# Performance work log

Measured on AMD Instinct MI355X. Metric: run time of the kernel, lower is better.

## Reference

```python
import jax, jax.numpy as jnp
import numpy as np
import math

B, TSRC, TTGT, DM, DI, H = 2, 2048, 2048, 1024, 1024, 16
DH = DI // H
LN_EPS = 1e-5


def setup_inputs() -> dict:
    key = jax.random.key(0)
    ks = iter(jax.random.split(key, 40))
    def p(*shape):
        return jax.random.normal(next(ks), shape, jnp.float32) * 0.02
    inp = {
        "enc_out_vecs": jax.random.normal(next(ks), (B, TSRC, DM), jnp.float32),
        "output_vecs": jax.random.normal(next(ks), (B, TTGT, DM), jnp.float32),
    }
    for tag in ("dd", "ed"):
        inp["Wq_" + tag] = p(DM, DI); inp["bq_" + tag] = jnp.zeros((DI,), jnp.float32)
        inp["Wk_" + tag] = p(DM, DI); inp["bk_" + tag] = jnp.zeros((DI,), jnp.float32)
        inp["Wv_" + tag] = p(DM, DI); inp["bv_" + tag] = jnp.zeros((DI,), jnp.float32)
        inp["Wo_" + tag] = p(DI, DM); inp["bo_" + tag] = jnp.zeros((DM,), jnp.float32)
        inp["W1_" + tag] = p(DM, 2 * DM); inp["b1_" + tag] = jnp.zeros((2 * DM,), jnp.float32)
        inp["W2_" + tag] = p(2 * DM, DM); inp["b2_" + tag] = jnp.zeros((DM,), jnp.float32)
        inp["g1_" + tag] = jnp.ones((DM,), jnp.float32); inp["be1_" + tag] = jnp.zeros((DM,), jnp.float32)
        inp["g2_" + tag] = jnp.ones((DM,), jnp.float32); inp["be2_" + tag] = jnp.zeros((DM,), jnp.float32)
    return inp


def _ln(x, g, b):
    m = jnp.mean(x, axis=-1, keepdims=True)
    v = jnp.var(x, axis=-1, keepdims=True)
    return (x - m) * jax.lax.rsqrt(v + LN_EPS) * g + b


def _mha(xq, xkv, Wq, bq, Wk, bk, Wv, bv, causal):
    Bb, Tq, _ = xq.shape
    Tk = xkv.shape[1]
    q = (xq @ Wq + bq).reshape(Bb, Tq, H, DH)
    k = (xkv @ Wk + bk).reshape(Bb, Tk, H, DH)
    v = (xkv @ Wv + bv).reshape(Bb, Tk, H, DH)
    s = jnp.einsum("bqhd,bkhd->bhqk", q, k) / math.sqrt(DH)
    if causal:
        mask = jnp.where(jnp.arange(Tk)[None, :] > jnp.arange(Tq)[:, None], -jnp.inf, 0.0)
        s = s + mask
    w = jax.nn.softmax(s, axis=-1)
    return jnp.einsum("bhqk,bkhd->bqhd", w, v).reshape(Bb, Tq, H * DH)


def reference(enc_out_vecs, output_vecs,
              Wq_dd, bq_dd, Wk_dd, bk_dd, Wv_dd, bv_dd, Wo_dd, bo_dd,
              W1_dd, b1_dd, W2_dd, b2_dd, g1_dd, be1_dd, g2_dd, be2_dd,
              Wq_ed, bq_ed, Wk_ed, bk_ed, Wv_ed, bv_ed, Wo_ed, bo_ed,
              W1_ed, b1_ed, W2_ed, b2_ed, g1_ed, be1_ed, g2_ed, be2_ed):
    # masked self-attention over decoder inputs
    x = output_vecs
    a = _mha(x, x, Wq_dd, bq_dd, Wk_dd, bk_dd, Wv_dd, bv_dd, causal=True)
    x = _ln(a @ Wo_dd + bo_dd + x, g1_dd, be1_dd)
    x = _ln(x + jax.nn.relu(x @ W1_dd + b1_dd) @ W2_dd + b2_dd, g2_dd, be2_dd)
    # cross attention against encoder outputs
    a = _mha(x, enc_out_vecs, Wq_ed, bq_ed, Wk_ed, bk_ed, Wv_ed, bv_ed, causal=False)
    x = _ln(a @ Wo_ed + bo_ed + x, g1_ed, be1_ed)
    x = _ln(jax.nn.relu(x @ W1_ed + b1_ed) @ W2_ed + b2_ed + x, g2_ed, be2_ed)
    return x
```

## Files before the change

kernel.cpp:

```cpp
#include <hip/hip_runtime.h>
#include <stdint.h>

#define DEV __device__ __forceinline__
typedef unsigned short u16;
typedef __attribute__((ext_vector_type(8))) short bf16x8;
typedef __attribute__((ext_vector_type(4))) float f32x4;

#define AS1 __attribute__((address_space(1)))
#define AS3 __attribute__((address_space(3)))
#define WAITVM0 asm volatile("s_waitcnt vmcnt(0)" ::: "memory")
#define QSCALE 0.18033688011112042f

DEV u16 f2bf(float f) {
  union { float f; uint32_t u; } x; x.f = f;
  uint32_t r = x.u + 0x7fffu + ((x.u >> 16) & 1u);
  return (u16)(r >> 16);
}

DEV float bf2f(u16 h) {
  union { uint32_t u; float f; } x; x.u = ((uint32_t)h) << 16;
  return x.f;
}

DEV uint32_t cvt_pk_bf16(float a, float b) {
  uint32_t r;
  asm("v_cvt_pk_bf16_f32 %0, %1, %2" : "=v"(r) : "v"(a), "v"(b));
  return r;
}

struct WTJob { const float* W; u16* WT; int K, M, msh, start; };
struct WTJobs { WTJob j[12]; };

__global__ __launch_bounds__(256) void k_init(WTJobs jobs, int wtBlocks,
                                              const float* __restrict__ a, const float* __restrict__ bsrc,
                                              u16* __restrict__ oa, u16* __restrict__ ob, int n4) {
  __shared__ float tile[32][33];
  int b = blockIdx.x;
  int tid = threadIdx.x;
  if (b >= wtBlocks) {
    int i = (b - wtBlocks) * 256 + tid;
    const float* s;
    u16* o;
    int k;
    if (i < n4) { s = a; o = oa; k = i; }
    else        { s = bsrc; o = ob; k = i - n4; }
    float4 v = reinterpret_cast<const float4*>(s)[k];
    reinterpret_cast<ushort4*>(o)[k] = make_ushort4(f2bf(v.x), f2bf(v.y), f2bf(v.z), f2bf(v.w));
    return;
  }
  int i = 0;
#pragma unroll
  for (int t = 1; t < 12; ++t)
    if (b >= jobs.j[t].start) i = t;
  const WTJob J = jobs.j[i];
  int rel = b - J.start;
  int m0 = (rel & ((1 << J.msh) - 1)) << 5;
  int k0 = (rel >> J.msh) << 5;
  int tx = tid & 31, ty = tid >> 5;
#pragma unroll
  for (int q = 0; q < 4; ++q)
    tile[ty + q * 8][tx] = J.W[(size_t)(k0 + ty + q * 8) * J.M + m0 + tx];
  __syncthreads();
#pragma unroll
  for (int q = 0; q < 4; ++q)
    J.WT[(size_t)(m0 + ty + q * 8) * J.K + k0 + tx] = f2bf(tile[tx][ty + q * 8]);
}

template<int R>
DEV void stage_tile(const u16* __restrict__ g, int strideElems, u16* lds, int tid, int wv) {
#pragma unroll
  for (int t = 0; t < R / 32; ++t) {
    int idx = t * 256 + tid;
    int row = idx >> 3;
    int b = (idx & 7) << 4;
    int sb = b ^ ((row & 7) << 4);
    const char* src = (const char*)g + (size_t)row * strideElems * 2 + sb;
    char* dst = (char*)lds + (size_t)(t * 256 + wv * 64) * 16;
    __builtin_amdgcn_global_load_lds((const AS1 void*)src, (AS3 void*)dst, 16, 0, 0);
  }
}

DEV bf16x8 lds_frag(const u16* lds, int row, int kel) {
  int off = row * 128 + ((kel * 2) ^ ((row & 7) << 4));
  return *(const bf16x8*)((const char*)lds + off);
}

template<int JT, int MODE>
__global__ __launch_bounds__(256) void k_gemm(const u16* __restrict__ A, int lda,
                                              const u16* __restrict__ BT,
                                              const float* __restrict__ bias,
                                              u16* __restrict__ C, int ldc, int K) {
  constexpr int BN = JT * 32;
  __shared__ __align__(16) u16 A_lds[2][128 * 64];
  __shared__ __align__(16) u16 B_lds[2][BN * 64];
  const int tid = threadIdx.x, lane = tid & 63, wv = tid >> 6;
  const int wm = wv >> 1, wn = wv & 1;
  const int nwg = gridDim.x * gridDim.y;
  const int flat = blockIdx.y * gridDim.x + blockIdx.x;
  const int sw = (flat & 7) * (nwg >> 3) + (flat >> 3);
  const int bx = sw % gridDim.x, by = sw / gridDim.x;
  const int bm0 = by * 128, bn0 = bx * BN;
  const int lr = lane & 15, lk = (lane >> 4) * 8, r0 = (lane >> 4) * 4;

  f32x4 acc[4][JT];
#pragma unroll
  for (int i = 0; i < 4; ++i)
#pragma unroll
    for (int j = 0; j < JT; ++j) acc[i][j] = f32x4{0.f, 0.f, 0.f, 0.f};

  stage_tile<128>(A + (size_t)bm0 * lda, lda, A_lds[0], tid, wv);
  stage_tile<BN>(BT + (size_t)bn0 * K, K, B_lds[0], tid, wv);
  WAITVM0;
  __builtin_amdgcn_s_barrier();

  int cur = 0;
  for (int k0 = 0; k0 < K; k0 += 64) {
    if (k0 + 64 < K) {
      stage_tile<128>(A + (size_t)bm0 * lda + k0 + 64, lda, A_lds[cur ^ 1], tid, wv);
      stage_tile<BN>(BT + (size_t)bn0 * K + k0 + 64, K, B_lds[cur ^ 1], tid, wv);
    }
#pragma unroll
    for (int kk = 0; kk < 2; ++kk) {
      bf16x8 af[4], bfr[JT];
#pragma unroll
      for (int i = 0; i < 4; ++i) af[i] = lds_frag(A_lds[cur], wm * 64 + i * 16 + lr, kk * 32 + lk);
#pragma unroll
      for (int j = 0; j < JT; ++j) bfr[j] = lds_frag(B_lds[cur], wn * (JT * 16) + j * 16 + lr, kk * 32 + lk);
#pragma unroll
      for (int i = 0; i < 4; ++i)
#pragma unroll
        for (int j = 0; j < JT; ++j)
          acc[i][j] = __builtin_amdgcn_mfma_f32_16x16x32_bf16(af[i], bfr[j], acc[i][j], 0, 0, 0);
    }
    WAITVM0;
    __builtin_amdgcn_s_barrier();
    cur ^= 1;
  }

#pragma unroll
  for (int j = 0; j < JT; ++j) {
    int col = bn0 + wn * (JT * 16) + j * 16 + lr;
    float bv = bias[col];
#pragma unroll
    for (int i = 0; i < 4; ++i) {
      int rowb = bm0 + wm * 64 + i * 16 + r0;
#pragma unroll
      for (int r = 0; r < 4; ++r) {
        float v = acc[i][j][r] + bv;
        if constexpr (MODE == 2) v = fmaxf(v, 0.f);
        C[(size_t)(rowb + r) * ldc + col] = f2bf(v);
      }
    }
  }
}

__global__ __launch_bounds__(256) void k_qkv(const u16* __restrict__ Aq, const u16* __restrict__ Akv,
                                             const u16* __restrict__ BT,
                                             const float* __restrict__ bq, const float* __restrict__ bk,
                                             const float* __restrict__ bv,
                                             u16* __restrict__ Qb, u16* __restrict__ Kb,
                                             u16* __restrict__ Vt, int K) {
  __shared__ __align__(16) u16 A_lds[2][128 * 64];
  __shared__ __align__(16) u16 B_lds[2][128 * 64];
  const int tid = threadIdx.x, lane = tid & 63, wv = tid >> 6;
  const int wm = wv >> 1, wn = wv & 1;
  const int nwg = gridDim.x * gridDim.y;
  const int flat = blockIdx.y * gridDim.x + blockIdx.x;
  const int sw = (flat & 7) * (nwg >> 3) + (flat >> 3);
  const int bx = sw % gridDim.x, by = sw / gridDim.x;
  const int bm0 = by * 128, bn0 = bx * 128;
  const int seg = bn0 >> 10;
  const u16* A = (seg == 0) ? Aq : Akv;
  const int lr = lane & 15, lk = (lane >> 4) * 8, r0 = (lane >> 4) * 4;

  f32x4 acc[4][4];
#pragma unroll
  for (int i = 0; i < 4; ++i)
#pragma unroll
    for (int j = 0; j < 4; ++j) acc[i][j] = f32x4{0.f, 0.f, 0.f, 0.f};

  stage_tile<128>(A + (size_t)bm0 * K, K, A_lds[0], tid, wv);
  stage_tile<128>(BT + (size_t)bn0 * K, K, B_lds[0], tid, wv);
  WAITVM0;
  __builtin_amdgcn_s_barrier();

  int cur = 0;
  for (int k0 = 0; k0 < K; k0 += 64) {
    if (k0 + 64 < K) {
      stage_tile<128>(A + (size_t)bm0 * K + k0 + 64, K, A_lds[cur ^ 1], tid, wv);
      stage_tile<128>(BT + (size_t)bn0 * K + k0 + 64, K, B_lds[cur ^ 1], tid, wv);
    }
#pragma unroll
    for (int kk = 0; kk < 2; ++kk) {
      bf16x8 af[4], bfr[4];
#pragma unroll
      for (int i = 0; i < 4; ++i) af[i] = lds_frag(A_lds[cur], wm * 64 + i * 16 + lr, kk * 32 + lk);
#pragma unroll
      for (int j = 0; j < 4; ++j) bfr[j] = lds_frag(B_lds[cur], wn * 64 + j * 16 + lr, kk * 32 + lk);
#pragma unroll
      for (int i = 0; i < 4; ++i)
#pragma unroll
        for (int j = 0; j < 4; ++j)
          acc[i][j] = __builtin_amdgcn_mfma_f32_16x16x32_bf16(af[i], bfr[j], acc[i][j], 0, 0, 0);
    }
    WAITVM0;
    __builtin_amdgcn_s_barrier();
    cur ^= 1;
  }

#pragma unroll
  for (int j = 0; j < 4; ++j) {
    int col = bn0 + wn * 64 + j * 16 + lr;
    int cl = col & 1023;
#pragma unroll
    for (int i = 0; i < 4; ++i) {
      int rowb = bm0 + wm * 64 + i * 16 + r0;
      if (seg == 0) {
        float bb = bq[cl];
#pragma unroll
        for (int r = 0; r < 4; ++r)
          Qb[(size_t)(rowb + r) * 1024 + cl] = f2bf((acc[i][j][r] + bb) * QSCALE);
      } else if (seg == 1) {
        float bb = bk[cl];
#pragma unroll
        for (int r = 0; r < 4; ++r)
          Kb[(size_t)(rowb + r) * 1024 + cl] = f2bf(acc[i][j][r] + bb);
      } else {
        float bb = bv[cl];
        int bidx = rowb >> 11, t = rowb & 2047;
        ushort4 o = make_ushort4(f2bf(acc[i][j][0] + bb), f2bf(acc[i][j][1] + bb),
                                 f2bf(acc[i][j][2] + bb), f2bf(acc[i][j][3] + bb));
        *reinterpret_cast<ushort4*>(&Vt[((size_t)bidx * 1024 + cl) * 2048 + t]) = o;
      }
    }
  }
}

__global__ __launch_bounds__(256) void k_ln_b(const u16* __restrict__ Rm, const u16* __restrict__ X,
                                              const float* __restrict__ g, const float* __restrict__ be,
                                              u16* __restrict__ Yb, float* __restrict__ Yf) {
  int row = blockIdx.x;
  size_t base4 = (size_t)row * 256;
  int t = threadIdx.x;
  ushort4 a4 = reinterpret_cast<const ushort4*>(Rm)[base4 + t];
  ushort4 x4 = reinterpret_cast<const ushort4*>(X)[base4 + t];
  float v0 = bf2f(a4.x) + bf2f(x4.x), v1 = bf2f(a4.y) + bf2f(x4.y);
  float v2 = bf2f(a4.z) + bf2f(x4.z), v3 = bf2f(a4.w) + bf2f(x4.w);
  float s = v0 + v1 + v2 + v3;
  float ss = v0 * v0 + v1 * v1 + v2 * v2 + v3 * v3;
#pragma unroll
  for (int m = 1; m < 64; m <<= 1) { s += __shfl_xor(s, m); ss += __shfl_xor(ss, m); }
  __shared__ float red[8];
  int wv = t >> 6;
  if ((t & 63) == 0) { red[wv] = s; red[4 + wv] = ss; }
  __syncthreads();
  s = red[0] + red[1] + red[2] + red[3];
  ss = red[4] + red[5] + red[6] + red[7];
  float mean = s * (1.f / 1024.f);
  float var = ss * (1.f / 1024.f) - mean * mean;
  float rstd = rsqrtf(var + 1e-5f);
  float4 gv = reinterpret_cast<const float4*>(g)[t];
  float4 bv = reinterpret_cast<const float4*>(be)[t];
  float o0 = (v0 - mean) * rstd * gv.x + bv.x;
  float o1 = (v1 - mean) * rstd * gv.y + bv.y;
  float o2 = (v2 - mean) * rstd * gv.z + bv.z;
  float o3 = (v3 - mean) * rstd * gv.w + bv.w;
  if (Yb) {
    ushort4 ob = make_ushort4(f2bf(o0), f2bf(o1), f2bf(o2), f2bf(o3));
    reinterpret_cast<ushort4*>(Yb)[base4 + t] = ob;
  }
  if (Yf)
    reinterpret_cast<float4*>(Yf)[base4 + t] = make_float4(o0, o1, o2, o3);
}

template<bool CAUSAL>
__global__ __launch_bounds__(512) void k_attn(const u16* __restrict__ Q, const u16* __restrict__ Kg,
                                              const u16* __restrict__ Vt, u16* __restrict__ O, int T) {
  __shared__ __align__(16) u16 K_lds[3][64 * 64];
  __shared__ __align__(16) u16 V_lds[3][64 * 64];
  __shared__ __align__(16) u16 p_lds[8][16 * 64];
  const int tid = threadIdx.x, lane = tid & 63, wv = tid >> 6;
  const int h = blockIdx.y, b = blockIdx.z;
  const int lq = lane & 15, g = lane >> 4;
  const int swz = (lq & 7) << 4;
  const int fb0 = lq * 128 + ((g * 16) ^ swz);
  const int fb1 = lq * 128 + ((g * 16 + 64) ^ swz);
  const size_t qkbase = ((size_t)b * T) * 1024 + h * 64;
  const size_t vbase = ((size_t)b * 1024 + h * 64) * T;

  const int qx = CAUSAL ? (gridDim.x - 1 - blockIdx.x) : blockIdx.x;
  const int en = CAUSAL ? (2 * qx + 2) : (T >> 6);
  const int qw = qx * 128 + wv * 16;
  const int dtile = qw >> 6;

  bf16x8 aq0, aq1;
  {
    const u16* qp_ = Q + qkbase + (size_t)(qw + lq) * 1024 + g * 8;
    aq0 = *reinterpret_cast<const bf16x8*>(qp_);
    aq1 = *reinterpret_cast<const bf16x8*>(qp_ + 32);
  }

  const int srow = tid >> 3;
  const int ssb = ((tid & 7) << 4) ^ ((srow & 7) << 4);
  const char* ksrc = (const char*)(Kg + qkbase) + (size_t)srow * 2048 + ssb;
  const char* vsrc = (const char*)(Vt + vbase) + (size_t)srow * ((size_t)T * 2) + ssb;
  const uint32_t doff = (uint32_t)(wv << 10);

  auto stage = [&](int buf) {
    __builtin_amdgcn_global_load_lds((const AS1 void*)ksrc, (AS3 void*)((char*)K_lds[buf] + doff), 16, 0, 0);
    __builtin_amdgcn_global_load_lds((const AS1 void*)vsrc, (AS3 void*)((char*)V_lds[buf] + doff), 16, 0, 0);
    ksrc += 131072;
    vsrc += 128;
  };

  f32x4 acc[4];
  float lsum = 0.f;
#pragma unroll
  for (int j = 0; j < 4; ++j) acc[j] = f32x4{0.f, 0.f, 0.f, 0.f};

  char* pw = (char*)p_lds[wv];

  auto qstep = [&](bool domask, int kv0, const char* kb, const char* vb) {
    f32x4 st_[4];
    __builtin_amdgcn_s_setprio(1);
#pragma unroll
    for (int j = 0; j < 4; ++j) {
      bf16x8 bk0 = *reinterpret_cast<const bf16x8*>(kb + fb0 + j * 2048);
      bf16x8 bk1 = *reinterpret_cast<const bf16x8*>(kb + fb1 + j * 2048);
      f32x4 t0 = f32x4{0.f, 0.f, 0.f, 0.f};
      t0 = __builtin_amdgcn_mfma_f32_16x16x32_bf16(bk0, aq0, t0, 0, 0, 0);
      t0 = __builtin_amdgcn_mfma_f32_16x16x32_bf16(bk1, aq1, t0, 0, 0, 0);
      st_[j] = t0;
    }
    __builtin_amdgcn_s_setprio(0);
    uint32_t pk[8];
    if (domask) {
      const int qrow = qw + lq;
#pragma unroll
      for (int j = 0; j < 4; ++j) {
        float p0 = __builtin_exp2f(st_[j][0]);
        float p1 = __builtin_exp2f(st_[j][1]);
        float p2 = __builtin_exp2f(st_[j][2]);
        float p3 = __builtin_exp2f(st_[j][3]);
        int kvb = kv0 + j * 16 + g * 4;
        p0 = (kvb > qrow) ? 0.f : p0;
        p1 = (kvb + 1 > qrow) ? 0.f : p1;
        p2 = (kvb + 2 > qrow) ? 0.f : p2;
        p3 = (kvb + 3 > qrow) ? 0.f : p3;
        lsum += (p0 + p1) + (p2 + p3);
        pk[2 * j] = cvt_pk_bf16(p0, p1);
        pk[2 * j + 1] = cvt_pk_bf16(p2, p3);
      }
    } else {
#pragma unroll
      for (int j = 0; j < 4; ++j) {
        float p0 = __builtin_exp2f(st_[j][0]);
        float p1 = __builtin_exp2f(st_[j][1]);
        float p2 = __builtin_exp2f(st_[j][2]);
        float p3 = __builtin_exp2f(st_[j][3]);
        lsum += (p0 + p1) + (p2 + p3);
        pk[2 * j] = cvt_pk_bf16(p0, p1);
        pk[2 * j + 1] = cvt_pk_bf16(p2, p3);
      }
    }
#pragma unroll
    for (int j = 0; j < 4; ++j)
      *reinterpret_cast<uint2*>(pw + lq * 128 + ((j * 32 + g * 8) ^ swz)) =
          make_uint2(pk[2 * j], pk[2 * j + 1]);
    bf16x8 pf0 = *reinterpret_cast<const bf16x8*>(pw + fb0);
    bf16x8 pf1 = *reinterpret_cast<const bf16x8*>(pw + fb1);
    __builtin_amdgcn_s_setprio(1);
#pragma unroll
    for (int j2 = 0; j2 < 4; ++j2) {
      bf16x8 v0 = *reinterpret_cast<const bf16x8*>(vb + fb0 + j2 * 2048);
      bf16x8 v1 = *reinterpret_cast<const bf16x8*>(vb + fb1 + j2 * 2048);
      acc[j2] = __builtin_amdgcn_mfma_f32_16x16x32_bf16(v0, pf0, acc[j2], 0, 0, 0);
      acc[j2] = __builtin_amdgcn_mfma_f32_16x16x32_bf16(v1, pf1, acc[j2], 0, 0, 0);
    }
    __builtin_amdgcn_s_setprio(0);
  };

  stage(0);
  if (en > 1) {
    stage(1);
    asm volatile("s_waitcnt vmcnt(2)" ::: "memory");
  } else {
    WAITVM0;
  }
  __builtin_amdgcn_s_barrier();

  for (int it = 0; it < en; ++it) {
    if (it + 2 < en) stage((it + 2) % 3);
    const char* kb = (const char*)K_lds[it % 3];
    const char* vb = (const char*)V_lds[it % 3];
    if (!CAUSAL || it <= dtile)
      qstep(CAUSAL && it == dtile, it << 6, kb, vb);
    if (it + 2 < en) {
      asm volatile("s_waitcnt vmcnt(2)" ::: "memory");
    } else {
      WAITVM0;
    }
    __builtin_amdgcn_s_barrier();
  }

  lsum += __shfl_xor(lsum, 16);
  lsum += __shfl_xor(lsum, 32);
  float inv = 1.f / lsum;
  size_t rb = qkbase + (size_t)(qw + lq) * 1024;
#pragma unroll
  for (int j2 = 0; j2 < 4; ++j2) {
    ushort4 o = make_ushort4(f2bf(acc[j2][0] * inv), f2bf(acc[j2][1] * inv),
                             f2bf(acc[j2][2] * inv), f2bf(acc[j2][3] * inv));
    *reinterpret_cast<ushort4*>(&O[rb + j2 * 16 + g * 4]) = o;
  }
}

extern "C" void kernel_launch(void* const* d_in, const int* in_sizes, int n_in,
                              void* d_out, int out_size, void* d_ws, size_t ws_size,
                              hipStream_t stream) {
  const int T = 2048;
  const float* enc = (const float*)d_in[0];
  const float* outv = (const float*)d_in[1];
  auto F = [&](int i) { return (const float*)d_in[i]; };

  size_t off = 0;
  auto alloc = [&](size_t bytes) {
    void* p = (char*)d_ws + off;
    off += (bytes + 255) & ~(size_t)255;
    return p;
  };

  const int tdK[12] = {1024, 1024, 1024, 1024, 1024, 2048, 1024, 1024, 1024, 1024, 1024, 2048};
  const int tdM[12] = {1024, 1024, 1024, 1024, 2048, 1024, 1024, 1024, 1024, 1024, 2048, 1024};
  const int tdIdx[12] = {2, 4, 6, 8, 10, 12, 18, 20, 22, 24, 26, 28};
  u16* WT_[12];
  for (int i = 0; i < 12; ++i) WT_[i] = (u16*)alloc((size_t)tdK[i] * tdM[i] * 2);

  u16* Xb0 = (u16*)alloc(4096ull * 1024 * 2);
  u16* Eb = (u16*)alloc(4096ull * 1024 * 2);
  u16* Qb = (u16*)alloc(4096ull * 1024 * 2);
  u16* Kb = (u16*)alloc(4096ull * 1024 * 2);
  u16* Vt = (u16*)alloc(4096ull * 1024 * 2);
  u16* Ab = (u16*)alloc(4096ull * 1024 * 2);
  u16* Hb = (u16*)alloc(4096ull * 2048 * 2);
  u16* Rm = (u16*)alloc(4096ull * 1024 * 2);
  u16* X1b = (u16*)alloc(4096ull * 1024 * 2);
  u16* X2b = (u16*)alloc(4096ull * 1024 * 2);
  u16* X3b = (u16*)alloc(4096ull * 1024 * 2);

  WTJobs jobs;
  int start = 0;
  for (int i = 0; i < 12; ++i) {
    int msh = (tdM[i] == 2048) ? 6 : 5;
    jobs.j[i] = {F(tdIdx[i]), WT_[i], tdK[i], tdM[i], msh, start};
    start += (tdM[i] >> 5) * (tdK[i] >> 5);
  }
  const int n4 = 4096 * 1024 / 4;
  k_init<<<start + 8192, 256, 0, stream>>>(jobs, start, outv, enc, Xb0, Eb, n4);

  dim3 gq(24, 32);
  dim3 g1k(16, 32);
  dim3 g2k(16, 32);
  dim3 ga(16, 16, 2);

  k_qkv<<<gq, 256, 0, stream>>>(Xb0, Xb0, WT_[0], F(3), F(5), F(7), Qb, Kb, Vt, 1024);
  k_attn<true><<<ga, 512, 0, stream>>>(Qb, Kb, Vt, Ab, T);
  k_gemm<2, 1><<<g1k, 256, 0, stream>>>(Ab, 1024, WT_[3], F(9), Rm, 1024, 1024);
  k_ln_b<<<4096, 256, 0, stream>>>(Rm, Xb0, F(14), F(15), X1b, nullptr);
  k_gemm<4, 2><<<g2k, 256, 0, stream>>>(X1b, 1024, WT_[4], F(11), Hb, 2048, 1024);
  k_gemm<2, 1><<<g1k, 256, 0, stream>>>(Hb, 2048, WT_[5], F(13), Rm, 1024, 2048);
  k_ln_b<<<4096, 256, 0, stream>>>(Rm, X1b, F(16), F(17), X2b, nullptr);

  k_qkv<<<gq, 256, 0, stream>>>(X2b, Eb, WT_[6], F(19), F(21), F(23), Qb, Kb, Vt, 1024);
  k_attn<false><<<ga, 512, 0, stream>>>(Qb, Kb, Vt, Ab, T);
  k_gemm<2, 1><<<g1k, 256, 0, stream>>>(Ab, 1024, WT_[9], F(25), Rm, 1024, 1024);
  k_ln_b<<<4096, 256, 0, stream>>>(Rm, X2b, F(30), F(31), X3b, nullptr);
  k_gemm<4, 2><<<g2k, 256, 0, stream>>>(X3b, 1024, WT_[10], F(27), Hb, 2048, 1024);
  k_gemm<2, 1><<<g1k, 256, 0, stream>>>(Hb, 2048, WT_[11], F(29), Rm, 1024, 2048);
  k_ln_b<<<4096, 256, 0, stream>>>(Rm, X3b, F(32), F(33), nullptr, (float*)d_out);
}
```

Before: 412.6 us.

## Overlap cross-attention K/V projection with causal self-attention in one launch

After: 396.9 us. -3.8%, faster.

```diff
diff --git a/kernel.cpp b/kernel.cpp
--- a/kernel.cpp
+++ b/kernel.cpp
@@ -80,6 +80,20 @@
   }
 }
 
+template<int R>
+DEV void stage512(const u16* __restrict__ g, int strideElems, u16* lds, int tid, int wv) {
+#pragma unroll
+  for (int t = 0; t < R / 64; ++t) {
+    int idx = t * 512 + tid;
+    int row = idx >> 3;
+    int b = (idx & 7) << 4;
+    int sb = b ^ ((row & 7) << 4);
+    const char* src = (const char*)g + (size_t)row * strideElems * 2 + sb;
+    char* dst = (char*)lds + (size_t)(t * 512 + wv * 64) * 16;
+    __builtin_amdgcn_global_load_lds((const AS1 void*)src, (AS3 void*)dst, 16, 0, 0);
+  }
+}
+
 DEV bf16x8 lds_frag(const u16* lds, int row, int kel) {
   int off = row * 128 + ((kel * 2) ^ ((row & 7) << 4));
   return *(const bf16x8*)((const char*)lds + off);
@@ -148,6 +162,7 @@
       for (int r = 0; r < 4; ++r) {
         float v = acc[i][j][r] + bv;
         if constexpr (MODE == 2) v = fmaxf(v, 0.f);
+        if constexpr (MODE == 3) v = v * QSCALE;
         C[(size_t)(rowb + r) * ldc + col] = f2bf(v);
       }
     }
@@ -415,6 +430,221 @@
   }
 }
 
+__global__ __launch_bounds__(512) void k_attn_kv(const u16* __restrict__ Q, const u16* __restrict__ Kg,
+                                                 const u16* __restrict__ Vt, u16* __restrict__ O, int T,
+                                                 const u16* __restrict__ Eb, const u16* __restrict__ BT2,
+                                                 const float* __restrict__ bk2, const float* __restrict__ bv2,
+                                                 u16* __restrict__ Kb2, u16* __restrict__ Vt2) {
+  __shared__ __align__(16) char smem[81920];
+  const int tid = threadIdx.x, lane = tid & 63, wv = tid >> 6;
+
+  if (blockIdx.x < 512) {
+    const int a = blockIdx.x;
+    const int b = a >> 8, h = (a >> 4) & 15, qi = a & 15;
+    const int qx = 15 - qi;
+    const int en = 2 * qx + 2;
+    const int lq = lane & 15, g = lane >> 4;
+    const int swz = (lq & 7) << 4;
+    const int fb0 = lq * 128 + ((g * 16) ^ swz);
+    const int fb1 = lq * 128 + ((g * 16 + 64) ^ swz);
+    const size_t qkbase = ((size_t)b * T) * 1024 + h * 64;
+    const size_t vbase = ((size_t)b * 1024 + h * 64) * T;
+    const int qw = qx * 128 + wv * 16;
+    const int dtile = qw >> 6;
+
+    char* Kl = smem;
+    char* Vl = smem + 24576;
+    char* pw = smem + 49152 + (wv << 11);
+
+    bf16x8 aq0, aq1;
+    {
+      const u16* qp_ = Q + qkbase + (size_t)(qw + lq) * 1024 + g * 8;
+      aq0 = *reinterpret_cast<const bf16x8*>(qp_);
+      aq1 = *reinterpret_cast<const bf16x8*>(qp_ + 32);
+    }
+
+    const int srow = tid >> 3;
+    const int ssb = ((tid & 7) << 4) ^ ((srow & 7) << 4);
+    const char* ksrc = (const char*)(Kg + qkbase) + (size_t)srow * 2048 + ssb;
+    const char* vsrc = (const char*)(Vt + vbase) + (size_t)srow * ((size_t)T * 2) + ssb;
+    const uint32_t doff = (uint32_t)(wv << 10);
+
+    auto stage = [&](int buf) {
+      __builtin_amdgcn_global_load_lds((const AS1 void*)ksrc, (AS3 void*)(Kl + buf * 8192 + doff), 16, 0, 0);
+      __builtin_amdgcn_global_load_lds((const AS1 void*)vsrc, (AS3 void*)(Vl + buf * 8192 + doff), 16, 0, 0);
+      ksrc += 131072;
+      vsrc += 128;
+    };
+
+    f32x4 acc[4];
+    float lsum = 0.f;
+#pragma unroll
+    for (int j = 0; j < 4; ++j) acc[j] = f32x4{0.f, 0.f, 0.f, 0.f};
+
+    auto qstep = [&](bool domask, int kv0, const char* kb, const char* vb) {
+      f32x4 st_[4];
+      __builtin_amdgcn_s_setprio(1);
+#pragma unroll
+      for (int j = 0; j < 4; ++j) {
+        bf16x8 bk0 = *reinterpret_cast<const bf16x8*>(kb + fb0 + j * 2048);
+        bf16x8 bk1 = *reinterpret_cast<const bf16x8*>(kb + fb1 + j * 2048);
+        f32x4 t0 = f32x4{0.f, 0.f, 0.f, 0.f};
+        t0 = __builtin_amdgcn_mfma_f32_16x16x32_bf16(bk0, aq0, t0, 0, 0, 0);
+        t0 = __builtin_amdgcn_mfma_f32_16x16x32_bf16(bk1, aq1, t0, 0, 0, 0);
+        st_[j] = t0;
+      }
+      __builtin_amdgcn_s_setprio(0);
+      uint32_t pk[8];
+      if (domask) {
+        const int qrow = qw + lq;
+#pragma unroll
+        for (int j = 0; j < 4; ++j) {
+          float p0 = __builtin_exp2f(st_[j][0]);
+          float p1 = __builtin_exp2f(st_[j][1]);
+          float p2 = __builtin_exp2f(st_[j][2]);
+          float p3 = __builtin_exp2f(st_[j][3]);
+          int kvb = kv0 + j * 16 + g * 4;
+          p0 = (kvb > qrow) ? 0.f : p0;
+          p1 = (kvb + 1 > qrow) ? 0.f : p1;
+          p2 = (kvb + 2 > qrow) ? 0.f : p2;
+          p3 = (kvb + 3 > qrow) ? 0.f : p3;
+          lsum += (p0 + p1) + (p2 + p3);
+          pk[2 * j] = cvt_pk_bf16(p0, p1);
+          pk[2 * j + 1] = cvt_pk_bf16(p2, p3);
+        }
+      } else {
+#pragma unroll
+        for (int j = 0; j < 4; ++j) {
+          float p0 = __builtin_exp2f(st_[j][0]);
+          float p1 = __builtin_exp2f(st_[j][1]);
+          float p2 = __builtin_exp2f(st_[j][2]);
+          float p3 = __builtin_exp2f(st_[j][3]);
+          lsum += (p0 + p1) + (p2 + p3);
+          pk[2 * j] = cvt_pk_bf16(p0, p1);
+          pk[2 * j + 1] = cvt_pk_bf16(p2, p3);
+        }
+      }
+#pragma unroll
+      for (int j = 0; j < 4; ++j)
+        *reinterpret_cast<uint2*>(pw + lq * 128 + ((j * 32 + g * 8) ^ swz)) =
+            make_uint2(pk[2 * j], pk[2 * j + 1]);
+      bf16x8 pf0 = *reinterpret_cast<const bf16x8*>(pw + fb0);
+      bf16x8 pf1 = *reinterpret_cast<const bf16x8*>(pw + fb1);
+      __builtin_amdgcn_s_setprio(1);
+#pragma unroll
+      for (int j2 = 0; j2 < 4; ++j2) {
+        bf16x8 v0 = *reinterpret_cast<const bf16x8*>(vb + fb0 + j2 * 2048);
+        bf16x8 v1 = *reinterpret_cast<const bf16x8*>(vb + fb1 + j2 * 2048);
+        acc[j2] = __builtin_amdgcn_mfma_f32_16x16x32_bf16(v0, pf0, acc[j2], 0, 0, 0);
+        acc[j2] = __builtin_amdgcn_mfma_f32_16x16x32_bf16(v1, pf1, acc[j2], 0, 0, 0);
+      }
+      __builtin_amdgcn_s_setprio(0);
+    };
+
+    stage(0);
+    if (en > 1) {
+      stage(1);
+      asm volatile("s_waitcnt vmcnt(2)" ::: "memory");
+    } else {
+      WAITVM0;
+    }
+    __builtin_amdgcn_s_barrier();
+
+    for (int it = 0; it < en; ++it) {
+      if (it + 2 < en) stage((it + 2) % 3);
+      const char* kb = Kl + (it % 3) * 8192;
+      const char* vb = Vl + (it % 3) * 8192;
+      if (it <= dtile)
+        qstep(it == dtile, it << 6, kb, vb);
+      if (it + 2 < en) {
+        asm volatile("s_waitcnt vmcnt(2)" ::: "memory");
+      } else {
+        WAITVM0;
+      }
+      __builtin_amdgcn_s_barrier();
+    }
+
+    lsum += __shfl_xor(lsum, 16);
+    lsum += __shfl_xor(lsum, 32);
+    float inv = 1.f / lsum;
+    size_t rb = qkbase + (size_t)(qw + lq) * 1024;
+#pragma unroll
+    for (int j2 = 0; j2 < 4; ++j2) {
+      ushort4 o = make_ushort4(f2bf(acc[j2][0] * inv), f2bf(acc[j2][1] * inv),
+                               f2bf(acc[j2][2] * inv), f2bf(acc[j2][3] * inv));
+      *reinterpret_cast<ushort4*>(&O[rb + j2 * 16 + g * 4]) = o;
+    }
+  } else {
+    const int g2 = blockIdx.x - 512;
+    const int bx = g2 & 31, by = g2 >> 5;
+    const int bm0 = by * 256, bn0 = bx * 64;
+    const int wm = wv >> 1, wn = wv & 1;
+    const int lr = lane & 15, lk = (lane >> 4) * 8, r0 = (lane >> 4) * 4;
+    u16* A_lds = (u16*)smem;
+    u16* B_lds = (u16*)(smem + 65536);
+    const int K = 1024;
+
+    f32x4 acc[4][2];
+#pragma unroll
+    for (int i = 0; i < 4; ++i)
+#pragma unroll
+      for (int j = 0; j < 2; ++j) acc[i][j] = f32x4{0.f, 0.f, 0.f, 0.f};
+
+    stage512<256>(Eb + (size_t)bm0 * K, K, A_lds, tid, wv);
+    stage512<64>(BT2 + (size_t)bn0 * K, K, B_lds, tid, wv);
+    WAITVM0;
+    __builtin_amdgcn_s_barrier();
+
+    int cur = 0;
+    for (int k0 = 0; k0 < K; k0 += 64) {
+      if (k0 + 64 < K) {
+        stage512<256>(Eb + (size_t)bm0 * K + k0 + 64, K, A_lds + (cur ^ 1) * 256 * 64, tid, wv);
+        stage512<64>(BT2 + (size_t)bn0 * K + k0 + 64, K, B_lds + (cur ^ 1) * 64 * 64, tid, wv);
+      }
+#pragma unroll
+      for (int kk = 0; kk < 2; ++kk) {
+        bf16x8 af[4], bfr[2];
+#pragma unroll
+        for (int i = 0; i < 4; ++i)
+          af[i] = lds_frag(A_lds + cur * 256 * 64, wm * 64 + i * 16 + lr, kk * 32 + lk);
+#pragma unroll
+        for (int j = 0; j < 2; ++j)
+          bfr[j] = lds_frag(B_lds + cur * 64 * 64, wn * 32 + j * 16 + lr, kk * 32 + lk);
+#pragma unroll
+        for (int i = 0; i < 4; ++i)
+#pragma unroll
+          for (int j = 0; j < 2; ++j)
+            acc[i][j] = __builtin_amdgcn_mfma_f32_16x16x32_bf16(af[i], bfr[j], acc[i][j], 0, 0, 0);
+      }
+      WAITVM0;
+      __builtin_amdgcn_s_barrier();
+      cur ^= 1;
+    }
+
+#pragma unroll
+    for (int j = 0; j < 2; ++j) {
+      int col = bn0 + wn * 32 + j * 16 + lr;
+#pragma unroll
+      for (int i = 0; i < 4; ++i) {
+        int rowb = bm0 + wm * 64 + i * 16 + r0;
+        if (col < 1024) {
+          float bb = bk2[col];
+#pragma unroll
+          for (int r = 0; r < 4; ++r)
+            Kb2[(size_t)(rowb + r) * 1024 + col] = f2bf(acc[i][j][r] + bb);
+        } else {
+          int cl = col - 1024;
+          float bb = bv2[cl];
+          int bidx = rowb >> 11, t = rowb & 2047;
+          ushort4 o = make_ushort4(f2bf(acc[i][j][0] + bb), f2bf(acc[i][j][1] + bb),
+                                   f2bf(acc[i][j][2] + bb), f2bf(acc[i][j][3] + bb));
+          *reinterpret_cast<ushort4*>(&Vt2[((size_t)bidx * 1024 + cl) * 2048 + t]) = o;
+        }
+      }
+    }
+  }
+}
+
 extern "C" void kernel_launch(void* const* d_in, const int* in_sizes, int n_in,
                               void* d_out, int out_size, void* d_ws, size_t ws_size,
                               hipStream_t stream) {
@@ -441,6 +671,9 @@
   u16* Qb = (u16*)alloc(4096ull * 1024 * 2);
   u16* Kb = (u16*)alloc(4096ull * 1024 * 2);
   u16* Vt = (u16*)alloc(4096ull * 1024 * 2);
+  u16* Qb2 = (u16*)alloc(4096ull * 1024 * 2);
+  u16* Kb2 = (u16*)alloc(4096ull * 1024 * 2);
+  u16* Vt2 = (u16*)alloc(4096ull * 1024 * 2);
   u16* Ab = (u16*)alloc(4096ull * 1024 * 2);
   u16* Hb = (u16*)alloc(4096ull * 2048 * 2);
   u16* Rm = (u16*)alloc(4096ull * 1024 * 2);
@@ -464,15 +697,15 @@
   dim3 ga(16, 16, 2);
 
   k_qkv<<<gq, 256, 0, stream>>>(Xb0, Xb0, WT_[0], F(3), F(5), F(7), Qb, Kb, Vt, 1024);
-  k_attn<true><<<ga, 512, 0, stream>>>(Qb, Kb, Vt, Ab, T);
+  k_attn_kv<<<1024, 512, 0, stream>>>(Qb, Kb, Vt, Ab, T, Eb, WT_[7], F(21), F(23), Kb2, Vt2);
   k_gemm<2, 1><<<g1k, 256, 0, stream>>>(Ab, 1024, WT_[3], F(9), Rm, 1024, 1024);
   k_ln_b<<<4096, 256, 0, stream>>>(Rm, Xb0, F(14), F(15), X1b, nullptr);
   k_gemm<4, 2><<<g2k, 256, 0, stream>>>(X1b, 1024, WT_[4], F(11), Hb, 2048, 1024);
   k_gemm<2, 1><<<g1k, 256, 0, stream>>>(Hb, 2048, WT_[5], F(13), Rm, 1024, 2048);
   k_ln_b<<<4096, 256, 0, stream>>>(Rm, X1b, F(16), F(17), X2b, nullptr);
 
-  k_qkv<<<gq, 256, 0, stream>>>(X2b, Eb, WT_[6], F(19), F(21), F(23), Qb, Kb, Vt, 1024);
-  k_attn<false><<<ga, 512, 0, stream>>>(Qb, Kb, Vt, Ab, T);
+  k_gemm<2, 3><<<g1k, 256, 0, stream>>>(X2b, 1024, WT_[6], F(19), Qb2, 1024, 1024);
+  k_attn<false><<<ga, 512, 0, stream>>>(Qb2, Kb2, Vt2, Ab, T);
   k_gemm<2, 1><<<g1k, 256, 0, stream>>>(Ab, 1024, WT_[9], F(25), Rm, 1024, 1024);
   k_ln_b<<<4096, 256, 0, stream>>>(Rm, X2b, F(30), F(31), X3b, nullptr);
   k_gemm<4, 2><<<g2k, 256, 0, stream>>>(X3b, 1024, WT_[10], F(27), Hb, 2048, 1024);
```
